# Kernel optimization log

Hardware: AMD Instinct MI355X
Metric: run time of the kernel (lower is better)

## Reference

```python
import jax, jax.numpy as jnp
import numpy as np

D = 8
W = 256
CX = 63   # in_channels_xyz
CD = 27   # in_channels_dir
CF = 3    # in_channels_fea
SKIPS = (4,)
B = 262144


def _linear_init(k, fin, fout):
    # matches torch nn.Linear default: U(-1/sqrt(fin), 1/sqrt(fin))
    k1, k2 = jax.random.split(k)
    s = 1.0 / np.sqrt(fin)
    w = jax.random.uniform(k1, (fin, fout), jnp.float32, -s, s)
    b = jax.random.uniform(k2, (fout,), jnp.float32, -s, s)
    return w, b


def setup_inputs() -> dict:
    key = jax.random.key(0)
    ks = jax.random.split(key, 16)
    inp = {"x": jax.random.normal(ks[0], (B, CX + CD + CF), jnp.float32)}
    for i in range(D):
        fin = CX if i == 0 else (W + CX if i in SKIPS else W)
        w, b = _linear_init(ks[1 + i], fin, W)
        inp[f"w{i}"] = w
        inp[f"b{i}"] = b
    inp["wf"], inp["bf"] = _linear_init(ks[10], W, W)                 # xyz_encoding_final
    inp["wd"], inp["bd"] = _linear_init(ks[11], W + CD + CF, W // 2)  # dir_encoding
    inp["ws"], inp["bs"] = _linear_init(ks[12], W, 1)                 # sigma head
    inp["wr"], inp["br"] = _linear_init(ks[13], W // 2, 3)            # rgb head
    return inp


def reference(x, w0, b0, w1, b1, w2, b2, w3, b3, w4, b4, w5, b5, w6, b6, w7, b7,
              wf, bf, wd, bd, ws, bs, wr, br):
    layers = [(w0, b0), (w1, b1), (w2, b2), (w3, b3),
              (w4, b4), (w5, b5), (w6, b6), (w7, b7)]
    input_xyz = x[:, :CX]            # (B, 63)
    dir_fea = x[:, CX:]              # (B, 30) = dir(27) + feature(3)
    h = input_xyz
    for i, (w, b) in enumerate(layers):
        if i in SKIPS:
            h = jnp.concatenate([input_xyz, h], axis=-1)
        h = jax.nn.relu(h @ w + b)   # (B, 256)
    sigma = h @ ws + bs              # (B, 1)
    xyz_final = h @ wf + bf          # (B, 256), no activation
    d = jax.nn.relu(jnp.concatenate([xyz_final, dir_fea], axis=-1) @ wd + bd)  # (B, 128)
    rgb = jax.nn.sigmoid(d @ wr + br)  # (B, 3)
    return jnp.concatenate([rgb, sigma], axis=-1)  # (B, 4)
```

## Files before the change

kernel.cpp:

```cpp
#include <hip/hip_runtime.h>

typedef __bf16  bf16x8 __attribute__((ext_vector_type(8)));
typedef float   f32x4  __attribute__((ext_vector_type(4)));
typedef unsigned int uint32x2 __attribute__((ext_vector_type(2)));

#define MFMA16(a,b,c) __builtin_amdgcn_mfma_f32_16x16x32_bf16((a),(b),(c),0,0,0)

template<int V> struct ic_t { static constexpr int value = V; };

enum : int {
    OFF_W0 = 0,
    OFF_W1 = OFF_W0 + 256 * 64,
    OFF_W2 = OFF_W1 + 256 * 256,
    OFF_W3 = OFF_W2 + 256 * 256,
    OFF_W4 = OFF_W3 + 256 * 256,
    OFF_W5 = OFF_W4 + 256 * 320,
    OFF_W6 = OFF_W5 + 256 * 256,
    OFF_W7 = OFF_W6 + 256 * 256,
    OFF_WF = OFF_W7 + 256 * 256,
    OFF_WD = OFF_WF + 256 * 256,
    W_TOTAL = OFF_WD + 128 * 288
};

__device__ __forceinline__ unsigned short f2bf(float f) {
    unsigned int u = __float_as_uint(f);
    u += 0x7FFFu + ((u >> 16) & 1u);
    return (unsigned short)(u >> 16);
}

__device__ __forceinline__ void prep_one(const float* __restrict__ src,
                                         unsigned short* __restrict__ dst,
                                         int fout, int Kp, int n1, int n2, int n3,
                                         int idx) {
    int n = idx / Kp;
    int k = idx - n * Kp;
    float v = 0.f;
    if (k < n1)                 v = src[k * fout + n];
    else if (k >= n2 && k < n3) v = src[(k - (n2 - n1)) * fout + n];
    dst[n * Kp + k] = f2bf(v);
}

__global__ void prep_kernel(const float* w0, const float* w1, const float* w2,
                            const float* w3, const float* w4, const float* w5,
                            const float* w6, const float* w7, const float* wf,
                            const float* wd, unsigned short* dst) {
    int i = blockIdx.x * 256 + threadIdx.x;
    if (i < 256 * 64)  { prep_one(w0, dst + OFF_W0, 256,  64,  63,  64,  64, i); return; }
    i -= 256 * 64;
    if (i < 256 * 256) { prep_one(w1, dst + OFF_W1, 256, 256, 256, 256, 256, i); return; }
    i -= 256 * 256;
    if (i < 256 * 256) { prep_one(w2, dst + OFF_W2, 256, 256, 256, 256, 256, i); return; }
    i -= 256 * 256;
    if (i < 256 * 256) { prep_one(w3, dst + OFF_W3, 256, 256, 256, 256, 256, i); return; }
    i -= 256 * 256;
    if (i < 256 * 320) { prep_one(w4, dst + OFF_W4, 256, 320,  63,  64, 320, i); return; }
    i -= 256 * 320;
    if (i < 256 * 256) { prep_one(w5, dst + OFF_W5, 256, 256, 256, 256, 256, i); return; }
    i -= 256 * 256;
    if (i < 256 * 256) { prep_one(w6, dst + OFF_W6, 256, 256, 256, 256, 256, i); return; }
    i -= 256 * 256;
    if (i < 256 * 256) { prep_one(w7, dst + OFF_W7, 256, 256, 256, 256, 256, i); return; }
    i -= 256 * 256;
    if (i < 256 * 256) { prep_one(wf, dst + OFF_WF, 256, 256, 256, 256, 256, i); return; }
    i -= 256 * 256;
    if (i < 128 * 288) { prep_one(wd, dst + OFF_WD, 128, 288, 286, 288, 288, i); return; }
}

struct Params {
    const float* x;
    const unsigned short* Wt;
    const float* b[8];
    const float* bfv;
    const float* bdv;
    const float* wsv;
    const float* bsv;
    const float* wrv;
    const float* brv;
    float* out;
};

__global__ __launch_bounds__(512, 2) void nerf_kernel(Params P) {
    __shared__ char Hs0[32768];
    __shared__ char Hs1[32768];
    __shared__ char Xs[8192];
    __shared__ char Ds[4096];

    const int t    = threadIdx.x;
    const int lane = t & 63;
    const int wave = t >> 6;
    const int lr   = lane & 15;
    const int lk   = lane >> 4;
    const int blockRow = blockIdx.x << 6;

    bf16x8 bp0[2], bp1[2], bp2[2];
    {
        const unsigned short* Wb0 = P.Wt + OFF_W0 + (size_t)((wave << 5) + lr) * 64 + (lk << 3);
#pragma unroll
        for (int nt = 0; nt < 2; ++nt) {
            bp0[nt] = *(const bf16x8*)(Wb0 + (size_t)(nt << 4) * 64);
            bp1[nt] = *(const bf16x8*)(Wb0 + (size_t)(nt << 4) * 64 + 32);
        }
    }

    {
        const float4* xb = (const float4*)(P.x + (size_t)blockRow * 93);
        for (int i = t; i < 1488; i += 512) {
            float4 v = xb[i];
            float vv[4] = {v.x, v.y, v.z, v.w};
#pragma unroll
            for (int j = 0; j < 4; ++j) {
                int e = (i << 2) + j;
                int r = e / 93;
                int c = e - r * 93;
                __bf16 us = (__bf16)vv[j];
                if (c < 63)
                    *(__bf16*)(Xs + ((r * 128 + c * 2) ^ ((r & 7) << 4))) = us;
                else
                    *(__bf16*)(Ds + ((r * 64 + (c - 63) * 2) ^ ((r & 3) << 4))) = us;
            }
        }
        if (t < 64) {
            int r = t;
            *(__bf16*)(Xs + ((r * 128 + 126) ^ ((r & 7) << 4))) = (__bf16)0.f;
            *(__bf16*)(Ds + ((r * 64 + 60) ^ ((r & 3) << 4))) = (__bf16)0.f;
            *(__bf16*)(Ds + ((r * 64 + 62) ^ ((r & 3) << 4))) = (__bf16)0.f;
        }
    }
    __syncthreads();

    auto ldH = [&](const char* B, int mt, int kt) -> bf16x8 {
        int row = (mt << 4) + lr;
        int off = (row * 512 + (kt << 6) + (lk << 4)) ^ ((row & 7) << 4);
        return *(const bf16x8*)(B + off);
    };
    auto ldXs = [&](int mt, int kt) -> bf16x8 {
        int row = (mt << 4) + lr;
        int off = (row * 128 + (kt << 6) + (lk << 4)) ^ ((row & 7) << 4);
        return *(const bf16x8*)(Xs + off);
    };
    auto ldDs = [&](int mt) -> bf16x8 {
        int row = (mt << 4) + lr;
        int off = (row * 64 + (lk << 4)) ^ ((row & 3) << 4);
        return *(const bf16x8*)(Ds + off);
    };

    auto gemm = [&](auto KTt, auto NTt, auto NTnt, auto&& getA,
                    const unsigned short* W, int Kp, const float* bias, bool dorelu,
                    char* dst, const unsigned short* Wn, int Kpn, int cbn) {
        constexpr int KT  = decltype(KTt)::value;
        constexpr int NT  = decltype(NTt)::value;
        constexpr int NTn = decltype(NTnt)::value;
        const int colbase = wave * (NT << 4);
        const unsigned short* Wb = W + (size_t)(colbase + lr) * Kp + (lk << 3);
        const unsigned short* Wbn = (NTn > 0) ? Wn + (size_t)(cbn + lr) * Kpn + (lk << 3) : nullptr;

        f32x4 acc[4][NT];
        {
            f32x4 bfr[NT];
#pragma unroll
            for (int nt = 0; nt < NT; ++nt)
                bfr[nt] = *(const f32x4*)(bias + colbase + (nt << 4) + (lk << 2));
#pragma unroll
            for (int mt = 0; mt < 4; ++mt)
#pragma unroll
                for (int nt = 0; nt < NT; ++nt) acc[mt][nt] = bfr[nt];
        }

        bf16x8 aC[4], aN[4];
#pragma unroll
        for (int mt = 0; mt < 4; ++mt) { aC[mt] = getA(mt, 0); aN[mt] = aC[mt]; }

#pragma unroll
        for (int kt = 0; kt < KT; ++kt) {
            if (kt + 2 < KT) {
#pragma unroll
                for (int nt = 0; nt < NT; ++nt)
                    bp2[nt] = *(const bf16x8*)(Wb + (size_t)(nt << 4) * Kp + ((kt + 2) << 5));
            } else if (NTn > 0) {
#pragma unroll
                for (int nt = 0; nt < (NTn > 0 ? NTn : 1); ++nt)
                    bp2[nt] = *(const bf16x8*)(Wbn + (size_t)(nt << 4) * Kpn + ((kt + 2 - KT) << 5));
            }
            if (kt + 1 < KT) {
#pragma unroll
                for (int mt = 0; mt < 4; ++mt) aN[mt] = getA(mt, kt + 1);
            }
            __builtin_amdgcn_s_setprio(1);
#pragma unroll
            for (int nt = 0; nt < NT; ++nt) {
#pragma unroll
                for (int mt = 0; mt < 4; ++mt)
                    acc[mt][nt] = MFMA16(bp0[nt], aC[mt], acc[mt][nt]);
            }
            __builtin_amdgcn_s_setprio(0);
#pragma unroll
            for (int nt = 0; nt < 2; ++nt) { bp0[nt] = bp1[nt]; bp1[nt] = bp2[nt]; }
#pragma unroll
            for (int mt = 0; mt < 4; ++mt) aC[mt] = aN[mt];
        }

#pragma unroll
        for (int nt = 0; nt < NT; ++nt) {
#pragma unroll
            for (int mt = 0; mt < 4; ++mt) {
                f32x4 v = acc[mt][nt];
                if (dorelu) {
#pragma unroll
                    for (int e = 0; e < 4; ++e) v[e] = fmaxf(v[e], 0.f);
                }
                unsigned int lo, hi;
                asm("v_cvt_pk_bf16_f32 %0, %1, %2" : "=v"(lo) : "v"(v[0]), "v"(v[1]));
                asm("v_cvt_pk_bf16_f32 %0, %1, %2" : "=v"(hi) : "v"(v[2]), "v"(v[3]));
                int batch = (mt << 4) + lr;
                int off = (batch * 512 + ((colbase + (nt << 4) + (lk << 2)) << 1)) ^ ((batch & 7) << 4);
                uint32x2 w2 = {lo, hi};
                *(uint32x2*)(dst + off) = w2;
            }
        }
    };

    const unsigned short* Wt = P.Wt;
    char* cur = Hs0;
    char* alt = Hs1;

    gemm(ic_t<2>{}, ic_t<2>{}, ic_t<2>{},
         [&](int mt, int kt) { return ldXs(mt, kt); },
         Wt + OFF_W0, 64, P.b[0], true, cur, Wt + OFF_W1, 256, wave << 5);
    __syncthreads();

    {
        const unsigned short* Wc[3] = {Wt + OFF_W1, Wt + OFF_W2, Wt + OFF_W3};
        const unsigned short* Wn[3] = {Wt + OFF_W2, Wt + OFF_W3, Wt + OFF_W4};
        const int Kpn[3] = {256, 256, 320};
        const float* bc[3] = {P.b[1], P.b[2], P.b[3]};
        for (int i = 0; i < 3; ++i) {
            gemm(ic_t<8>{}, ic_t<2>{}, ic_t<2>{},
                 [&](int mt, int kt) { return ldH(cur, mt, kt); },
                 Wc[i], 256, bc[i], true, alt, Wn[i], Kpn[i], wave << 5);
            __syncthreads();
            char* tmp = cur; cur = alt; alt = tmp;
        }
    }

    gemm(ic_t<10>{}, ic_t<2>{}, ic_t<2>{},
         [&](int mt, int kt) { return (kt < 2) ? ldXs(mt, kt) : ldH(cur, mt, kt - 2); },
         Wt + OFF_W4, 320, P.b[4], true, alt, Wt + OFF_W5, 256, wave << 5);
    __syncthreads();
    { char* tmp = cur; cur = alt; alt = tmp; }

    {
        const unsigned short* Wc[3] = {Wt + OFF_W5, Wt + OFF_W6, Wt + OFF_W7};
        const unsigned short* Wn[3] = {Wt + OFF_W6, Wt + OFF_W7, Wt + OFF_WF};
        const float* bc[3] = {P.b[5], P.b[6], P.b[7]};
        for (int i = 0; i < 3; ++i) {
            gemm(ic_t<8>{}, ic_t<2>{}, ic_t<2>{},
                 [&](int mt, int kt) { return ldH(cur, mt, kt); },
                 Wc[i], 256, bc[i], true, alt, Wn[i], 256, wave << 5);
            __syncthreads();
            char* tmp = cur; cur = alt; alt = tmp;
        }
    }

    float sig;
    {
        int rr = t >> 3, q = t & 7;
        float sp = 0.f;
#pragma unroll
        for (int j = 0; j < 4; ++j) {
            int cb = (q << 5) + (j << 3);
            bf16x8 h8 = *(const bf16x8*)(cur + ((rr * 512 + (cb << 1)) ^ ((rr & 7) << 4)));
#pragma unroll
            for (int e = 0; e < 8; ++e) sp += (float)h8[e] * P.wsv[cb + e];
        }
        sp += __shfl_xor(sp, 1);
        sp += __shfl_xor(sp, 2);
        sp += __shfl_xor(sp, 4);
        sig = sp + P.bsv[0];
    }

    gemm(ic_t<8>{}, ic_t<2>{}, ic_t<1>{},
         [&](int mt, int kt) { return ldH(cur, mt, kt); },
         Wt + OFF_WF, 256, P.bfv, false, alt, Wt + OFF_WD, 288, wave << 4);
    __syncthreads();
    { char* tmp = cur; cur = alt; alt = tmp; }

    gemm(ic_t<9>{}, ic_t<1>{}, ic_t<0>{},
         [&](int mt, int kt) { return (kt < 8) ? ldH(cur, mt, kt) : ldDs(mt); },
         Wt + OFF_WD, 288, P.bdv, true, alt, nullptr, 0, 0);
    __syncthreads();

    {
        int rr = t >> 3, q = t & 7;
        float c0 = 0.f, c1 = 0.f, c2 = 0.f;
#pragma unroll
        for (int j = 0; j < 2; ++j) {
            int kb = (q << 4) + (j << 3);
            bf16x8 d8 = *(const bf16x8*)(alt + ((rr * 512 + (kb << 1)) ^ ((rr & 7) << 4)));
#pragma unroll
            for (int e = 0; e < 8; ++e) {
                float dv = (float)d8[e];
                const float* w = P.wrv + (kb + e) * 3;
                c0 += dv * w[0]; c1 += dv * w[1]; c2 += dv * w[2];
            }
        }
        c0 += __shfl_xor(c0, 1); c0 += __shfl_xor(c0, 2); c0 += __shfl_xor(c0, 4);
        c1 += __shfl_xor(c1, 1); c1 += __shfl_xor(c1, 2); c1 += __shfl_xor(c1, 4);
        c2 += __shfl_xor(c2, 1); c2 += __shfl_xor(c2, 2); c2 += __shfl_xor(c2, 4);
        if (q == 0) {
            float4 o;
            o.x = 1.f / (1.f + __expf(-(c0 + P.brv[0])));
            o.y = 1.f / (1.f + __expf(-(c1 + P.brv[1])));
            o.z = 1.f / (1.f + __expf(-(c2 + P.brv[2])));
            o.w = sig;
            ((float4*)P.out)[blockRow + rr] = o;
        }
    }
}

extern "C" void kernel_launch(void* const* d_in, const int* in_sizes, int n_in,
                              void* d_out, int out_size, void* d_ws, size_t ws_size,
                              hipStream_t stream) {
    const float* x = (const float*)d_in[0];
    const float* w[8];
    const float* b[8];
    for (int i = 0; i < 8; ++i) {
        w[i] = (const float*)d_in[1 + 2 * i];
        b[i] = (const float*)d_in[2 + 2 * i];
    }
    const float* wf  = (const float*)d_in[17];
    const float* bfv = (const float*)d_in[18];
    const float* wd  = (const float*)d_in[19];
    const float* bdv = (const float*)d_in[20];
    const float* wsv = (const float*)d_in[21];
    const float* bsv = (const float*)d_in[22];
    const float* wrv = (const float*)d_in[23];
    const float* brv = (const float*)d_in[24];

    unsigned short* Wt = (unsigned short*)d_ws;

    prep_kernel<<<(W_TOTAL + 255) / 256, 256, 0, stream>>>(
        w[0], w[1], w[2], w[3], w[4], w[5], w[6], w[7], wf, wd, Wt);

    Params P;
    P.x = x; P.Wt = Wt;
    for (int i = 0; i < 8; ++i) P.b[i] = b[i];
    P.bfv = bfv; P.bdv = bdv; P.wsv = wsv; P.bsv = bsv; P.wrv = wrv; P.brv = brv;
    P.out = (float*)d_out;

    nerf_kernel<<<262144 / 64, 512, 0, stream>>>(P);
}
```

Measured before the change: 622.2 us.

## Deepen weight prefetch pipeline and use LDS-only barriers between layers

The per-layer GEMM now keeps three k-tiles of weight fragments in flight instead of two. The first three k-tiles of the next layer's weights are loaded right after the k-loop, before the epilogue, rather than inside the last two iterations. All __syncthreads calls become an s_waitcnt lgkmcnt(0) plus s_barrier, so in-flight global weight loads no longer have to drain at each layer boundary. This aims to hide global-load latency across layer transitions, at the cost of extra VGPRs for the deeper prefetch buffer and reliance on LDS-only ordering being sufficient.

```diff
diff --git a/kernel.cpp b/kernel.cpp
--- a/kernel.cpp
+++ b/kernel.cpp
@@ -28,6 +28,11 @@
     return (unsigned short)(u >> 16);
 }
 
+__device__ __forceinline__ void soft_barrier() {
+    asm volatile("s_waitcnt lgkmcnt(0)" ::: "memory");
+    __builtin_amdgcn_s_barrier();
+}
+
 __device__ __forceinline__ void prep_one(const float* __restrict__ src,
                                          unsigned short* __restrict__ dst,
                                          int fout, int Kp, int n1, int n2, int n3,
@@ -99,6 +104,7 @@
         for (int nt = 0; nt < 2; ++nt) {
             bp0[nt] = *(const bf16x8*)(Wb0 + (size_t)(nt << 4) * 64);
             bp1[nt] = *(const bf16x8*)(Wb0 + (size_t)(nt << 4) * 64 + 32);
+            bp2[nt] = bp1[nt];
         }
     }
 
@@ -126,7 +132,7 @@
             *(__bf16*)(Ds + ((r * 64 + 62) ^ ((r & 3) << 4))) = (__bf16)0.f;
         }
     }
-    __syncthreads();
+    soft_barrier();
 
     auto ldH = [&](const char* B, int mt, int kt) -> bf16x8 {
         int row = (mt << 4) + lr;
@@ -152,7 +158,6 @@
         constexpr int NTn = decltype(NTnt)::value;
         const int colbase = wave * (NT << 4);
         const unsigned short* Wb = W + (size_t)(colbase + lr) * Kp + (lk << 3);
-        const unsigned short* Wbn = (NTn > 0) ? Wn + (size_t)(cbn + lr) * Kpn + (lk << 3) : nullptr;
 
         f32x4 acc[4][NT];
         {
@@ -172,14 +177,13 @@
 
 #pragma unroll
         for (int kt = 0; kt < KT; ++kt) {
-            if (kt + 2 < KT) {
-#pragma unroll
-                for (int nt = 0; nt < NT; ++nt)
-                    bp2[nt] = *(const bf16x8*)(Wb + (size_t)(nt << 4) * Kp + ((kt + 2) << 5));
-            } else if (NTn > 0) {
-#pragma unroll
-                for (int nt = 0; nt < (NTn > 0 ? NTn : 1); ++nt)
-                    bp2[nt] = *(const bf16x8*)(Wbn + (size_t)(nt << 4) * Kpn + ((kt + 2 - KT) << 5));
+            bf16x8 bpN[2];
+#pragma unroll
+            for (int nt = 0; nt < NT; ++nt) {
+                if (kt + 3 < KT)
+                    bpN[nt] = *(const bf16x8*)(Wb + (size_t)(nt << 4) * Kp + ((kt + 3) << 5));
+                else
+                    bpN[nt] = bp2[nt];
             }
             if (kt + 1 < KT) {
 #pragma unroll
@@ -194,9 +198,19 @@
             }
             __builtin_amdgcn_s_setprio(0);
 #pragma unroll
-            for (int nt = 0; nt < 2; ++nt) { bp0[nt] = bp1[nt]; bp1[nt] = bp2[nt]; }
+            for (int nt = 0; nt < 2; ++nt) { bp0[nt] = bp1[nt]; bp1[nt] = bp2[nt]; bp2[nt] = bpN[nt]; }
 #pragma unroll
             for (int mt = 0; mt < 4; ++mt) aC[mt] = aN[mt];
+        }
+
+        if (NTn > 0) {
+            const unsigned short* Wbn = Wn + (size_t)(cbn + lr) * Kpn + (lk << 3);
+#pragma unroll
+            for (int nt = 0; nt < (NTn > 0 ? NTn : 1); ++nt) {
+                bp0[nt] = *(const bf16x8*)(Wbn + (size_t)(nt << 4) * Kpn);
+                bp1[nt] = *(const bf16x8*)(Wbn + (size_t)(nt << 4) * Kpn + 32);
+                bp2[nt] = *(const bf16x8*)(Wbn + (size_t)(nt << 4) * Kpn + 64);
+            }
         }
 
 #pragma unroll
@@ -226,7 +240,7 @@
     gemm(ic_t<2>{}, ic_t<2>{}, ic_t<2>{},
          [&](int mt, int kt) { return ldXs(mt, kt); },
          Wt + OFF_W0, 64, P.b[0], true, cur, Wt + OFF_W1, 256, wave << 5);
-    __syncthreads();
+    soft_barrier();
 
     {
         const unsigned short* Wc[3] = {Wt + OFF_W1, Wt + OFF_W2, Wt + OFF_W3};
@@ -237,7 +251,7 @@
             gemm(ic_t<8>{}, ic_t<2>{}, ic_t<2>{},
                  [&](int mt, int kt) { return ldH(cur, mt, kt); },
                  Wc[i], 256, bc[i], true, alt, Wn[i], Kpn[i], wave << 5);
-            __syncthreads();
+            soft_barrier();
             char* tmp = cur; cur = alt; alt = tmp;
         }
     }
@@ -245,7 +259,7 @@
     gemm(ic_t<10>{}, ic_t<2>{}, ic_t<2>{},
          [&](int mt, int kt) { return (kt < 2) ? ldXs(mt, kt) : ldH(cur, mt, kt - 2); },
          Wt + OFF_W4, 320, P.b[4], true, alt, Wt + OFF_W5, 256, wave << 5);
-    __syncthreads();
+    soft_barrier();
     { char* tmp = cur; cur = alt; alt = tmp; }
 
     {
@@ -256,7 +270,7 @@
             gemm(ic_t<8>{}, ic_t<2>{}, ic_t<2>{},
                  [&](int mt, int kt) { return ldH(cur, mt, kt); },
                  Wc[i], 256, bc[i], true, alt, Wn[i], 256, wave << 5);
-            __syncthreads();
+            soft_barrier();
             char* tmp = cur; cur = alt; alt = tmp;
         }
     }
@@ -281,13 +295,13 @@
     gemm(ic_t<8>{}, ic_t<2>{}, ic_t<1>{},
          [&](int mt, int kt) { return ldH(cur, mt, kt); },
          Wt + OFF_WF, 256, P.bfv, false, alt, Wt + OFF_WD, 288, wave << 4);
-    __syncthreads();
+    soft_barrier();
     { char* tmp = cur; cur = alt; alt = tmp; }
 
     gemm(ic_t<9>{}, ic_t<1>{}, ic_t<0>{},
          [&](int mt, int kt) { return (kt < 8) ? ldH(cur, mt, kt) : ldDs(mt); },
          Wt + OFF_WD, 288, P.bdv, true, alt, nullptr, 0, 0);
-    __syncthreads();
+    soft_barrier();
 
     {
         int rr = t >> 3, q = t & 7;
```

After: 614.4 us. No clear change (-1.3%).
